# Performance work log

Measured on AMD Instinct MI355X. Metric: run time of the kernel, lower is better.

## Reference

```python
import jax, jax.numpy as jnp
import numpy as np
import math

HEADS = 12

def setup_inputs() -> dict:
    key = jax.random.key(0)
    ks = jax.random.split(key, 5)
    E = 768
    r, i, n = 64, 256, 2
    s = 0.02  # init scale for weights
    return {
        "x": jax.random.normal(ks[0], (r, i, n, E), dtype=jnp.float32),
        "Wq": jax.random.normal(ks[1], (E, E), dtype=jnp.float32) * s,
        "bq": jnp.zeros((E,), dtype=jnp.float32),
        "Wk": jax.random.normal(ks[2], (E, E), dtype=jnp.float32) * s,
        "bk": jnp.zeros((E,), dtype=jnp.float32),
        "Wv": jax.random.normal(ks[3], (E, E), dtype=jnp.float32) * s,
        "bv": jnp.zeros((E,), dtype=jnp.float32),
        "Wo": jax.random.normal(ks[4], (E, E), dtype=jnp.float32) * s,
        "bo": jnp.zeros((E,), dtype=jnp.float32),
    }


def reference(x, Wq, bq, Wk, bk, Wv, bv, Wo, bo):
    r, i, n, E = x.shape
    h = HEADS
    d = E // h
    shape = (r, i, n, h, d)
    q = (x @ Wq + bq).reshape(shape)
    k = (x @ Wk + bk).reshape(shape)
    v = (x @ Wv + bv).reshape(shape)
    # tied row attention: 1/sqrt(d) softmax scale plus 1/sqrt(num_rows) for row sum
    scaling = d ** (-0.5) / math.sqrt(r)
    q = q * scaling
    # scores shared across all rows: contract over row axis r and head dim d
    attn_weights = jnp.einsum('rinhd,rjnhd->hnij', q, k)  # [h, n, i, j]
    attn_probs = jax.nn.softmax(attn_weights, axis=-1)
    # dropout disabled (deterministic=True)
    context = jnp.einsum('hnij,rjnhd->rinhd', attn_probs, v)
    context = context.reshape(r, i, n, E)
    return context @ Wo + bo
```

## Files before the change

kernel.cpp:

```cpp
#include <hip/hip_runtime.h>
#include <stdint.h>

typedef __attribute__((ext_vector_type(8))) short bf16x8;
typedef __attribute__((ext_vector_type(4))) float f32x4;
typedef __attribute__((ext_vector_type(4))) unsigned short us4;
typedef __attribute__((ext_vector_type(8))) unsigned short us8;

static __device__ __forceinline__ unsigned short f2bf(float f) {
  union { float f; unsigned u; } c; c.f = f;
  unsigned r = c.u + 0x7fffu + ((c.u >> 16) & 1u);
  return (unsigned short)(r >> 16);
}

#define LDP 80

__device__ __forceinline__ void gemm_core(
    const unsigned short* __restrict__ Ag, int lda,
    const unsigned short* __restrict__ Bg, int ldb,
    int K, unsigned short* As, unsigned short* Bs, f32x4 acc[4][4])
{
  const int tid  = threadIdx.x;
  const int lane = tid & 63;
  const int wid  = tid >> 6;
  const int wr = wid >> 1, wc = wid & 1;
  const int lr = lane & 15, kg = lane >> 4;

  for (int kt = 0; kt < K; kt += 64) {
    us8 av[4], bv[4];
#pragma unroll
    for (int c = 0; c < 4; ++c) {
      int idx = c * 256 + tid, row = idx >> 3, ch = idx & 7;
      av[c] = *reinterpret_cast<const us8*>(Ag + row * lda + kt + ch * 8);
      bv[c] = *reinterpret_cast<const us8*>(Bg + row * ldb + kt + ch * 8);
    }
    __syncthreads();
#pragma unroll
    for (int c = 0; c < 4; ++c) {
      int idx = c * 256 + tid, row = idx >> 3, ch = idx & 7;
      *reinterpret_cast<us8*>(As + row * LDP + ch * 8) = av[c];
      *reinterpret_cast<us8*>(Bs + row * LDP + ch * 8) = bv[c];
    }
    __syncthreads();
#pragma unroll
    for (int ks = 0; ks < 2; ++ks) {
      bf16x8 af[4], bfr[4];
#pragma unroll
      for (int mi = 0; mi < 4; ++mi)
        af[mi] = *reinterpret_cast<const bf16x8*>(As + (wr*64 + mi*16 + lr) * LDP + ks*32 + kg*8);
#pragma unroll
      for (int ni = 0; ni < 4; ++ni)
        bfr[ni] = *reinterpret_cast<const bf16x8*>(Bs + (wc*64 + ni*16 + lr) * LDP + ks*32 + kg*8);
#pragma unroll
      for (int mi = 0; mi < 4; ++mi)
#pragma unroll
        for (int ni = 0; ni < 4; ++ni)
          acc[mi][ni] = __builtin_amdgcn_mfma_f32_16x16x32_bf16(af[mi], bfr[ni], acc[mi][ni], 0, 0, 0);
    }
  }
}

#define ACC_ZERO(acc) do { \
  f32x4 z = {0.f, 0.f, 0.f, 0.f}; \
  for (int a_ = 0; a_ < 4; ++a_) for (int b_ = 0; b_ < 4; ++b_) acc[a_][b_] = z; } while (0)

#define EPI_VARS \
  int tid = threadIdx.x, lane = tid & 63, wid = tid >> 6; \
  int wr = wid >> 1, wc = wid & 1, lr = lane & 15, kg = lane >> 4; (void)wr; (void)wc;

#define GEMM_LDS \
  __shared__ unsigned short As[128 * LDP], Bs[128 * LDP];


__global__ __launch_bounds__(256) void k_cvt_x(const float* __restrict__ x,
                                               unsigned short* __restrict__ xb) {
  int i = blockIdx.x * 256 + threadIdx.x;
  f32x4 f = reinterpret_cast<const f32x4*>(x)[i];
  us4 o = { f2bf(f[0]), f2bf(f[1]), f2bf(f[2]), f2bf(f[3]) };
  reinterpret_cast<us4*>(xb)[i] = o;
}

__global__ __launch_bounds__(256) void k_cvt_w(
    const float* __restrict__ Wq, const float* __restrict__ Wk, const float* __restrict__ Wv,
    const float* __restrict__ Wo, const float* __restrict__ bq, const float* __restrict__ bk,
    const float* __restrict__ bv, unsigned short* __restrict__ wT,
    unsigned short* __restrict__ woT, float* __restrict__ bqkv)
{
  const float qs = 1.0f / 64.0f;
  int o = blockIdx.x * 256 + threadIdx.x;
  if (o < 2304 * 768) {
    int col = o / 768, k = o % 768;
    float v;
    if (col < 768)       v = Wq[k * 768 + col] * qs;
    else if (col < 1536) v = Wk[k * 768 + col - 768];
    else                 v = Wv[k * 768 + col - 1536];
    wT[o] = f2bf(v);
  } else if (o < 2304 * 768 + 768 * 768) {
    int o2 = o - 2304 * 768;
    int col = o2 / 768, k = o2 % 768;
    woT[o2] = f2bf(Wo[k * 768 + col]);
  } else {
    int o3 = o - (2304 * 768 + 768 * 768);
    float v = (o3 < 768) ? bq[o3] * qs : (o3 < 1536 ? bk[o3 - 768] : bv[o3 - 1536]);
    bqkv[o3] = v;
  }
}

__global__ __launch_bounds__(256) void k_gemm_qkv(
    const unsigned short* __restrict__ xb, const unsigned short* __restrict__ wT,
    const float* __restrict__ bqkv, unsigned short* __restrict__ qkvb)
{
  GEMM_LDS;
  int bx = blockIdx.x, bn = bx % 18, bm = bx / 18;
  f32x4 acc[4][4]; ACC_ZERO(acc);
  gemm_core(xb + (size_t)bm * 128 * 768, 768, wT + (size_t)bn * 128 * 768, 768, 768, As, Bs, acc);
  EPI_VARS;
#pragma unroll
  for (int mi = 0; mi < 4; ++mi)
#pragma unroll
    for (int ni = 0; ni < 4; ++ni) {
      int col = bn * 128 + wc * 64 + ni * 16 + lr;
      float bias = bqkv[col];
#pragma unroll
      for (int e = 0; e < 4; ++e) {
        int row = bm * 128 + wr * 64 + mi * 16 + kg * 4 + e;
        qkvb[(size_t)row * 2304 + col] = f2bf(acc[mi][ni][e] + bias);
      }
    }
}

__global__ __launch_bounds__(256) void k_repack_v(
    const unsigned short* __restrict__ qkvb, unsigned short* __restrict__ V)
{
  __shared__ unsigned short lds[64 * LDP];
  int bx = blockIdx.x;
  int jt = bx & 3, rr = (bx >> 2) & 63, hn = bx >> 8;
  int h = hn >> 1, nn = hn & 1;
  int t = threadIdx.x;
  int j = t >> 3, ch = t & 7;
#pragma unroll
  for (int p = 0; p < 2; ++p) {
    int jj = p * 32 + j;
    us8 v = *reinterpret_cast<const us8*>(
        qkvb + ((size_t)((rr * 256 + jt * 64 + jj) * 2 + nn)) * 2304 + 1536 + h * 64 + ch * 8);
#pragma unroll
    for (int e = 0; e < 8; ++e) lds[(ch * 8 + e) * LDP + jj] = v[e];
  }
  __syncthreads();
  int dd = t >> 2, cj = t & 3;
  size_t ob = ((size_t)(hn * 64 + rr) * 64) * 256;
#pragma unroll
  for (int p = 0; p < 2; ++p) {
    int c2 = cj + p * 4;
    us8 v = *reinterpret_cast<const us8*>(lds + dd * LDP + c2 * 8);
    *reinterpret_cast<us8*>(V + ob + (size_t)dd * 256 + jt * 64 + c2 * 8) = v;
  }
}

__global__ __launch_bounds__(256) void k_gemm_scores(
    const unsigned short* __restrict__ qkvb, float* __restrict__ Spart)
{
  GEMM_LDS;
  int bx = blockIdx.x;
  int s = bx / 96, rblk = bx % 96;
  int hn = rblk >> 2, tt = rblk & 3, bm = tt >> 1, bn = tt & 1;
  int h = hn >> 1, nn = hn & 1;
  const int hq = h * 64;
  f32x4 acc[4][4]; ACC_ZERO(acc);

  const int tid = threadIdx.x, lane = tid & 63, wid = tid >> 6;
  const int wr = wid >> 1, wc = wid & 1, lr = lane & 15, kg = lane >> 4;
  const int srow = tid >> 3, sch = tid & 7;

  for (int t = 0; t < 16; ++t) {
    int rr = s * 16 + t;
    us8 av[4], bv[4];
#pragma unroll
    for (int c = 0; c < 4; ++c) {
      int row = c * 32 + srow;
      size_t ab = ((size_t)((rr * 256 + bm * 128 + row) * 2 + nn)) * 2304 + hq + sch * 8;
      size_t bb = ((size_t)((rr * 256 + bn * 128 + row) * 2 + nn)) * 2304 + 768 + hq + sch * 8;
      av[c] = *reinterpret_cast<const us8*>(qkvb + ab);
      bv[c] = *reinterpret_cast<const us8*>(qkvb + bb);
    }
    __syncthreads();
#pragma unroll
    for (int c = 0; c < 4; ++c) {
      int row = c * 32 + srow;
      *reinterpret_cast<us8*>(As + row * LDP + sch * 8) = av[c];
      *reinterpret_cast<us8*>(Bs + row * LDP + sch * 8) = bv[c];
    }
    __syncthreads();
#pragma unroll
    for (int ks = 0; ks < 2; ++ks) {
      bf16x8 af[4], bfr[4];
#pragma unroll
      for (int mi = 0; mi < 4; ++mi)
        af[mi] = *reinterpret_cast<const bf16x8*>(As + (wr*64 + mi*16 + lr) * LDP + ks*32 + kg*8);
#pragma unroll
      for (int ni = 0; ni < 4; ++ni)
        bfr[ni] = *reinterpret_cast<const bf16x8*>(Bs + (wc*64 + ni*16 + lr) * LDP + ks*32 + kg*8);
#pragma unroll
      for (int mi = 0; mi < 4; ++mi)
#pragma unroll
        for (int ni = 0; ni < 4; ++ni)
          acc[mi][ni] = __builtin_amdgcn_mfma_f32_16x16x32_bf16(af[mi], bfr[ni], acc[mi][ni], 0, 0, 0);
    }
  }

  float* Ss = Spart + ((size_t)s * 24 + hn) * 65536;
#pragma unroll
  for (int mi = 0; mi < 4; ++mi)
#pragma unroll
    for (int ni = 0; ni < 4; ++ni)
#pragma unroll
      for (int e = 0; e < 4; ++e) {
        int row = bm * 128 + wr * 64 + mi * 16 + kg * 4 + e;
        int col = bn * 128 + wc * 64 + ni * 16 + lr;
        Ss[(size_t)row * 256 + col] = acc[mi][ni][e];
      }
}

__global__ __launch_bounds__(256) void k_softmax(const float* __restrict__ Sp,
                                                 unsigned short* __restrict__ P)
{
  __shared__ float red[8];
  size_t row = blockIdx.x;
  int t = threadIdx.x, wid = t >> 6, lane = t & 63;
  size_t idx = row * 256 + t;
  float v = Sp[idx] + Sp[idx + 1572864] + Sp[idx + 2 * 1572864] + Sp[idx + 3 * 1572864];
  float m = v;
#pragma unroll
  for (int o = 32; o; o >>= 1) m = fmaxf(m, __shfl_xor(m, o));
  if (lane == 0) red[wid] = m;
  __syncthreads();
  m = fmaxf(fmaxf(red[0], red[1]), fmaxf(red[2], red[3]));
  float e = __expf(v - m);
  float sm = e;
#pragma unroll
  for (int o = 32; o; o >>= 1) sm += __shfl_xor(sm, o);
  if (lane == 0) red[4 + wid] = sm;
  __syncthreads();
  sm = red[4] + red[5] + red[6] + red[7];
  P[row * 256 + t] = f2bf(e / sm);
}

__global__ __launch_bounds__(256) void k_gemm_ctx(
    const unsigned short* __restrict__ P, const unsigned short* __restrict__ V,
    unsigned short* __restrict__ Cb)
{
  GEMM_LDS;
  int bx = blockIdx.x;
  int hn = bx / 64, tt = bx % 64, bm = tt >> 5, bn = tt & 31;
  f32x4 acc[4][4]; ACC_ZERO(acc);
  const unsigned short* Ag = P + (size_t)hn * 65536 + (size_t)bm * 128 * 256;
  const unsigned short* Bg = V + (size_t)hn * 4096 * 256 + (size_t)bn * 128 * 256;
  gemm_core(Ag, 256, Bg, 256, 256, As, Bs, acc);
  EPI_VARS;
  int nn = hn & 1;
  int h = hn >> 1;
#pragma unroll
  for (int mi = 0; mi < 4; ++mi)
#pragma unroll
    for (int ni = 0; ni < 4; ++ni) {
      int c = bn * 128 + wc * 64 + ni * 16 + lr;
      int rr = c >> 6, dd = c & 63;
#pragma unroll
      for (int e = 0; e < 4; ++e) {
        int i = bm * 128 + wr * 64 + mi * 16 + kg * 4 + e;
        int tok = (rr * 256 + i) * 2 + nn;
        Cb[(size_t)tok * 768 + h * 64 + dd] = f2bf(acc[mi][ni][e]);
      }
    }
}

__global__ __launch_bounds__(256) void k_gemm_out(
    const unsigned short* __restrict__ Cb, const unsigned short* __restrict__ woT,
    const float* __restrict__ bo, float* __restrict__ out)
{
  GEMM_LDS;
  int b0 = blockIdx.x;
  int bx = (b0 & 7) * 192 + (b0 >> 3);
  int bn = bx % 6, bm = bx / 6;
  f32x4 acc[4][4]; ACC_ZERO(acc);
  gemm_core(Cb + (size_t)bm * 128 * 768, 768, woT + (size_t)bn * 128 * 768, 768, 768, As, Bs, acc);
  EPI_VARS;
#pragma unroll
  for (int mi = 0; mi < 4; ++mi)
#pragma unroll
    for (int ni = 0; ni < 4; ++ni) {
      int col = bn * 128 + wc * 64 + ni * 16 + lr;
      float bias = bo[col];
#pragma unroll
      for (int e = 0; e < 4; ++e) {
        int row = bm * 128 + wr * 64 + mi * 16 + kg * 4 + e;
        out[(size_t)row * 768 + col] = acc[mi][ni][e] + bias;
      }
    }
}

extern "C" void kernel_launch(void* const* d_in, const int* in_sizes, int n_in,
                              void* d_out, int out_size, void* d_ws, size_t ws_size,
                              hipStream_t stream)
{
  const float* x  = (const float*)d_in[0];
  const float* Wq = (const float*)d_in[1];
  const float* bq = (const float*)d_in[2];
  const float* Wk = (const float*)d_in[3];
  const float* bk = (const float*)d_in[4];
  const float* Wv = (const float*)d_in[5];
  const float* bv = (const float*)d_in[6];
  const float* Wo = (const float*)d_in[7];
  const float* bo = (const float*)d_in[8];
  float* out = (float*)d_out;

  char* ws = (char*)d_ws;
  size_t off = 0;
  auto alloc = [&](size_t bytes) { void* p = ws + off; off += (bytes + 255) & ~(size_t)255; return p; };
  unsigned short* xb   = (unsigned short*)alloc(50331648);
  unsigned short* qkvb = (unsigned short*)alloc(150994944);
  unsigned short* Vb   = (unsigned short*)alloc(50331648);
  unsigned short* Cb   = (unsigned short*)alloc(50331648);
  unsigned short* wT   = (unsigned short*)alloc(3538944);
  unsigned short* woT  = (unsigned short*)alloc(1179648);
  float*          bqkv = (float*)alloc(9216);
  if (off > ws_size) return;

  float*          Sp = (float*)d_out;
  unsigned short* P  = (unsigned short*)((char*)d_out + 25165824);

  k_cvt_x      <<<24576, 256, 0, stream>>>(x, xb);
  k_cvt_w      <<<9225,  256, 0, stream>>>(Wq, Wk, Wv, Wo, bq, bk, bv, wT, woT, bqkv);
  k_gemm_qkv   <<<4608,  256, 0, stream>>>(xb, wT, bqkv, qkvb);
  k_repack_v   <<<6144,  256, 0, stream>>>(qkvb, Vb);
  k_gemm_scores<<<384,   256, 0, stream>>>(qkvb, Sp);
  k_softmax    <<<6144,  256, 0, stream>>>(Sp, P);
  k_gemm_ctx   <<<1536,  256, 0, stream>>>(P, Vb, Cb);
  k_gemm_out   <<<1536,  256, 0, stream>>>(Cb, woT, bo, out);
}
```

Baseline: 347.9 us.

## Fuse fp32-to-bf16 conversion of x into the QKV GEMM tile loads

Removes the separate x conversion kernel and its bf16 workspace buffer. The QKV GEMM now loads fp32 x directly, converts it to bf16 in registers and writes it into LDS. It also remaps block indices so that groups of consecutive blocks spread across the grid, likely for cache or XCD locality. In exchange, each A tile is read from global memory at twice the bytes and converted again, once for each of the 18 column blocks that reuse it.

New measurement: 403.0 us. +15.8%, slower.

```diff
diff --git a/kernel.cpp b/kernel.cpp
--- a/kernel.cpp
+++ b/kernel.cpp
@@ -70,14 +70,6 @@
 #define GEMM_LDS \
   __shared__ unsigned short As[128 * LDP], Bs[128 * LDP];
 
-
-__global__ __launch_bounds__(256) void k_cvt_x(const float* __restrict__ x,
-                                               unsigned short* __restrict__ xb) {
-  int i = blockIdx.x * 256 + threadIdx.x;
-  f32x4 f = reinterpret_cast<const f32x4*>(x)[i];
-  us4 o = { f2bf(f[0]), f2bf(f[1]), f2bf(f[2]), f2bf(f[3]) };
-  reinterpret_cast<us4*>(xb)[i] = o;
-}
 
 __global__ __launch_bounds__(256) void k_cvt_w(
     const float* __restrict__ Wq, const float* __restrict__ Wk, const float* __restrict__ Wv,
@@ -106,14 +98,60 @@
 }
 
 __global__ __launch_bounds__(256) void k_gemm_qkv(
-    const unsigned short* __restrict__ xb, const unsigned short* __restrict__ wT,
+    const float* __restrict__ x, const unsigned short* __restrict__ wT,
     const float* __restrict__ bqkv, unsigned short* __restrict__ qkvb)
 {
   GEMM_LDS;
-  int bx = blockIdx.x, bn = bx % 18, bm = bx / 18;
+  int b0 = blockIdx.x;
+  int bx = (b0 & 7) * 576 + (b0 >> 3);
+  int bn = bx % 18, bm = bx / 18;
+
+  const int tid = threadIdx.x, lane = tid & 63, wid = tid >> 6;
+  const int wr = wid >> 1, wc = wid & 1, lr = lane & 15, kg = lane >> 4;
+  const int srow = tid >> 3, sch = tid & 7;
+
+  const float* Ax = x + (size_t)bm * 128 * 768;
+  const unsigned short* Bg = wT + (size_t)bn * 128 * 768;
   f32x4 acc[4][4]; ACC_ZERO(acc);
-  gemm_core(xb + (size_t)bm * 128 * 768, 768, wT + (size_t)bn * 128 * 768, 768, 768, As, Bs, acc);
-  EPI_VARS;
+
+  for (int kt = 0; kt < 768; kt += 64) {
+    f32x4 a0[4], a1[4]; us8 bv[4];
+#pragma unroll
+    for (int c = 0; c < 4; ++c) {
+      int row = c * 32 + srow;
+      const float* ap = Ax + (size_t)row * 768 + kt + sch * 8;
+      a0[c] = *reinterpret_cast<const f32x4*>(ap);
+      a1[c] = *reinterpret_cast<const f32x4*>(ap + 4);
+      bv[c] = *reinterpret_cast<const us8*>(Bg + row * 768 + kt + sch * 8);
+    }
+    __syncthreads();
+#pragma unroll
+    for (int c = 0; c < 4; ++c) {
+      int row = c * 32 + srow;
+      us8 a;
+      a[0] = f2bf(a0[c][0]); a[1] = f2bf(a0[c][1]); a[2] = f2bf(a0[c][2]); a[3] = f2bf(a0[c][3]);
+      a[4] = f2bf(a1[c][0]); a[5] = f2bf(a1[c][1]); a[6] = f2bf(a1[c][2]); a[7] = f2bf(a1[c][3]);
+      *reinterpret_cast<us8*>(As + row * LDP + sch * 8) = a;
+      *reinterpret_cast<us8*>(Bs + row * LDP + sch * 8) = bv[c];
+    }
+    __syncthreads();
+#pragma unroll
+    for (int ks = 0; ks < 2; ++ks) {
+      bf16x8 af[4], bfr[4];
+#pragma unroll
+      for (int mi = 0; mi < 4; ++mi)
+        af[mi] = *reinterpret_cast<const bf16x8*>(As + (wr*64 + mi*16 + lr) * LDP + ks*32 + kg*8);
+#pragma unroll
+      for (int ni = 0; ni < 4; ++ni)
+        bfr[ni] = *reinterpret_cast<const bf16x8*>(Bs + (wc*64 + ni*16 + lr) * LDP + ks*32 + kg*8);
+#pragma unroll
+      for (int mi = 0; mi < 4; ++mi)
+#pragma unroll
+        for (int ni = 0; ni < 4; ++ni)
+          acc[mi][ni] = __builtin_amdgcn_mfma_f32_16x16x32_bf16(af[mi], bfr[ni], acc[mi][ni], 0, 0, 0);
+    }
+  }
+
 #pragma unroll
   for (int mi = 0; mi < 4; ++mi)
 #pragma unroll
@@ -316,7 +354,6 @@
   char* ws = (char*)d_ws;
   size_t off = 0;
   auto alloc = [&](size_t bytes) { void* p = ws + off; off += (bytes + 255) & ~(size_t)255; return p; };
-  unsigned short* xb   = (unsigned short*)alloc(50331648);
   unsigned short* qkvb = (unsigned short*)alloc(150994944);
   unsigned short* Vb   = (unsigned short*)alloc(50331648);
   unsigned short* Cb   = (unsigned short*)alloc(50331648);
@@ -328,9 +365,8 @@
   float*          Sp = (float*)d_out;
   unsigned short* P  = (unsigned short*)((char*)d_out + 25165824);
 
-  k_cvt_x      <<<24576, 256, 0, stream>>>(x, xb);
   k_cvt_w      <<<9225,  256, 0, stream>>>(Wq, Wk, Wv, Wo, bq, bk, bv, wT, woT, bqkv);
-  k_gemm_qkv   <<<4608,  256, 0, stream>>>(xb, wT, bqkv, qkvb);
+  k_gemm_qkv   <<<4608,  256, 0, stream>>>(x, wT, bqkv, qkvb);
   k_repack_v   <<<6144,  256, 0, stream>>>(qkvb, Vb);
   k_gemm_scores<<<384,   256, 0, stream>>>(qkvb, Sp);
   k_softmax    <<<6144,  256, 0, stream>>>(Sp, P);
```

## Double-buffer GEMM core with direct global-to-LDS loads and XOR swizzle

Applied to the files above, without the earlier changes.

The shared GEMM core now loads tiles straight from global memory into LDS with global_load_lds instead of staging them through registers. Two LDS buffers let the next K tile load while the current one is computed. An XOR swizzle on the 16-byte chunk index replaces the padded row stride to avoid bank conflicts. LDS use for the GEMM kernels doubles, which may lower occupancy, and the scores kernel keeps its own padded single-buffer layout.

New measurement: 352.6 us. Within noise of the previous version (+1.3%).

```diff
diff --git a/kernel.cpp b/kernel.cpp
--- a/kernel.cpp
+++ b/kernel.cpp
@@ -12,7 +12,50 @@
   return (unsigned short)(r >> 16);
 }
 
+static __device__ __forceinline__ void gl_lds16(const unsigned short* g, unsigned short* l) {
+  __builtin_amdgcn_global_load_lds(
+      (const __attribute__((address_space(1))) unsigned int*)g,
+      (__attribute__((address_space(3))) unsigned int*)l, 16, 0, 0);
+}
+
 #define LDP 80
+
+__device__ __forceinline__ void stage8(
+    const unsigned short* __restrict__ Ag, int lda,
+    const unsigned short* __restrict__ Bg, int ldb, int kt,
+    unsigned short* As, unsigned short* Bs, int tid, int wid)
+{
+#pragma unroll
+  for (int c = 0; c < 4; ++c) {
+    int chunk = c * 256 + tid;
+    int row = chunk >> 3, u = chunk & 7;
+    int ch = u ^ (row & 7);
+    gl_lds16(Ag + row * lda + kt + ch * 8, As + ((c * 256 + wid * 64) << 3));
+    gl_lds16(Bg + row * ldb + kt + ch * 8, Bs + ((c * 256 + wid * 64) << 3));
+  }
+}
+
+__device__ __forceinline__ void compute64(
+    const unsigned short* As, const unsigned short* Bs, f32x4 acc[4][4],
+    int wr, int wc, int lr, int kg, int l7)
+{
+#pragma unroll
+  for (int ks = 0; ks < 2; ++ks) {
+    bf16x8 af[4], bfr[4];
+    int u = (ks * 4 + kg) ^ l7;
+#pragma unroll
+    for (int mi = 0; mi < 4; ++mi)
+      af[mi] = *reinterpret_cast<const bf16x8*>(As + (wr*64 + mi*16 + lr) * 64 + u * 8);
+#pragma unroll
+    for (int ni = 0; ni < 4; ++ni)
+      bfr[ni] = *reinterpret_cast<const bf16x8*>(Bs + (wc*64 + ni*16 + lr) * 64 + u * 8);
+#pragma unroll
+    for (int mi = 0; mi < 4; ++mi)
+#pragma unroll
+      for (int ni = 0; ni < 4; ++ni)
+        acc[mi][ni] = __builtin_amdgcn_mfma_f32_16x16x32_bf16(af[mi], bfr[ni], acc[mi][ni], 0, 0, 0);
+  }
+}
 
 __device__ __forceinline__ void gemm_core(
     const unsigned short* __restrict__ Ag, int lda,
@@ -24,39 +67,23 @@
   const int wid  = tid >> 6;
   const int wr = wid >> 1, wc = wid & 1;
   const int lr = lane & 15, kg = lane >> 4;
-
-  for (int kt = 0; kt < K; kt += 64) {
-    us8 av[4], bv[4];
-#pragma unroll
-    for (int c = 0; c < 4; ++c) {
-      int idx = c * 256 + tid, row = idx >> 3, ch = idx & 7;
-      av[c] = *reinterpret_cast<const us8*>(Ag + row * lda + kt + ch * 8);
-      bv[c] = *reinterpret_cast<const us8*>(Bg + row * ldb + kt + ch * 8);
-    }
-    __syncthreads();
-#pragma unroll
-    for (int c = 0; c < 4; ++c) {
-      int idx = c * 256 + tid, row = idx >> 3, ch = idx & 7;
-      *reinterpret_cast<us8*>(As + row * LDP + ch * 8) = av[c];
-      *reinterpret_cast<us8*>(Bs + row * LDP + ch * 8) = bv[c];
-    }
-    __syncthreads();
-#pragma unroll
-    for (int ks = 0; ks < 2; ++ks) {
-      bf16x8 af[4], bfr[4];
-#pragma unroll
-      for (int mi = 0; mi < 4; ++mi)
-        af[mi] = *reinterpret_cast<const bf16x8*>(As + (wr*64 + mi*16 + lr) * LDP + ks*32 + kg*8);
-#pragma unroll
-      for (int ni = 0; ni < 4; ++ni)
-        bfr[ni] = *reinterpret_cast<const bf16x8*>(Bs + (wc*64 + ni*16 + lr) * LDP + ks*32 + kg*8);
-#pragma unroll
-      for (int mi = 0; mi < 4; ++mi)
-#pragma unroll
-        for (int ni = 0; ni < 4; ++ni)
-          acc[mi][ni] = __builtin_amdgcn_mfma_f32_16x16x32_bf16(af[mi], bfr[ni], acc[mi][ni], 0, 0, 0);
-    }
-  }
+  const int l7 = lane & 7;
+
+  const int nt = K >> 6;
+  stage8(Ag, lda, Bg, ldb, 0, As, Bs, tid, wid);
+  int cur = 0;
+  for (int t = 0; t < nt - 1; ++t) {
+    stage8(Ag, lda, Bg, ldb, (t + 1) << 6,
+           As + (cur ^ 1) * 8192, Bs + (cur ^ 1) * 8192, tid, wid);
+    asm volatile("s_waitcnt vmcnt(8)" ::: "memory");
+    __builtin_amdgcn_s_barrier();
+    compute64(As + cur * 8192, Bs + cur * 8192, acc, wr, wc, lr, kg, l7);
+    __builtin_amdgcn_s_barrier();
+    cur ^= 1;
+  }
+  asm volatile("s_waitcnt vmcnt(0)" ::: "memory");
+  __builtin_amdgcn_s_barrier();
+  compute64(As + cur * 8192, Bs + cur * 8192, acc, wr, wc, lr, kg, l7);
 }
 
 #define ACC_ZERO(acc) do { \
@@ -68,7 +95,7 @@
   int wr = wid >> 1, wc = wid & 1, lr = lane & 15, kg = lane >> 4; (void)wr; (void)wc;
 
 #define GEMM_LDS \
-  __shared__ unsigned short As[128 * LDP], Bs[128 * LDP];
+  __shared__ unsigned short As[2 * 128 * 64], Bs[2 * 128 * 64];
 
 
 __global__ __launch_bounds__(256) void k_cvt_x(const float* __restrict__ x,
@@ -159,7 +186,7 @@
 __global__ __launch_bounds__(256) void k_gemm_scores(
     const unsigned short* __restrict__ qkvb, float* __restrict__ Spart)
 {
-  GEMM_LDS;
+  __shared__ unsigned short Asp[128 * LDP], Bsp[128 * LDP];
   int bx = blockIdx.x;
   int s = bx / 96, rblk = bx % 96;
   int hn = rblk >> 2, tt = rblk & 3, bm = tt >> 1, bn = tt & 1;
@@ -186,8 +213,8 @@
 #pragma unroll
     for (int c = 0; c < 4; ++c) {
       int row = c * 32 + srow;
-      *reinterpret_cast<us8*>(As + row * LDP + sch * 8) = av[c];
-      *reinterpret_cast<us8*>(Bs + row * LDP + sch * 8) = bv[c];
+      *reinterpret_cast<us8*>(Asp + row * LDP + sch * 8) = av[c];
+      *reinterpret_cast<us8*>(Bsp + row * LDP + sch * 8) = bv[c];
     }
     __syncthreads();
 #pragma unroll
@@ -195,10 +222,10 @@
       bf16x8 af[4], bfr[4];
 #pragma unroll
       for (int mi = 0; mi < 4; ++mi)
-        af[mi] = *reinterpret_cast<const bf16x8*>(As + (wr*64 + mi*16 + lr) * LDP + ks*32 + kg*8);
+        af[mi] = *reinterpret_cast<const bf16x8*>(Asp + (wr*64 + mi*16 + lr) * LDP + ks*32 + kg*8);
 #pragma unroll
       for (int ni = 0; ni < 4; ++ni)
-        bfr[ni] = *reinterpret_cast<const bf16x8*>(Bs + (wc*64 + ni*16 + lr) * LDP + ks*32 + kg*8);
+        bfr[ni] = *reinterpret_cast<const bf16x8*>(Bsp + (wc*64 + ni*16 + lr) * LDP + ks*32 + kg*8);
 #pragma unroll
       for (int mi = 0; mi < 4; ++mi)
 #pragma unroll
```
